# Performance work log

Hardware: AMD Instinct MI355X
Metric: run time of the kernel (lower is better)

## Reference

```python
import jax, jax.numpy as jnp
import numpy as np

N = 50000
E = 800000
G_DIM = 128
HEADS = 8
DEPTH = 3
EPS = 1e-5


def _ln(x, w, b):
    m = jnp.mean(x, axis=-1, keepdims=True)
    v = jnp.var(x, axis=-1, keepdims=True)
    return (x - m) * jax.lax.rsqrt(v + EPS) * w + b


def setup_inputs() -> dict:
    key = jax.random.key(0)
    ks = jax.random.split(key, 12)
    s = 0.02
    inp = {
        "h": jax.random.normal(ks[0], (N, G_DIM), jnp.float32),
        "src": jax.random.randint(ks[1], (E,), 0, N, jnp.int32),
        "dst": jax.random.randint(ks[2], (E,), 0, N, jnp.int32),
        # outer norm
        "norm_w": jnp.ones((G_DIM,), jnp.float32),
        "norm_b": jnp.zeros((G_DIM,), jnp.float32),
        # attention norm_in
        "nin_w": jnp.ones((G_DIM,), jnp.float32),
        "nin_b": jnp.zeros((G_DIM,), jnp.float32),
        # to_qkv (no bias)
        "Wqkv": jax.random.normal(ks[3], (G_DIM, 3 * G_DIM), jnp.float32) * s,
        # ff norm_out
        "no_w": jnp.ones((G_DIM,), jnp.float32),
        "no_b": jnp.zeros((G_DIM,), jnp.float32),
        # ff linears (hidden = 4*g_dim)
        "W1": jax.random.normal(ks[4], (G_DIM, 4 * G_DIM), jnp.float32) * s,
        "b1": jnp.zeros((4 * G_DIM,), jnp.float32),
        "W2": jax.random.normal(ks[5], (4 * G_DIM, G_DIM), jnp.float32) * s,
        "b2": jnp.zeros((G_DIM,), jnp.float32),
    }
    return inp


def _graph_attention(x, src, dst, nin_w, nin_b, Wqkv):
    # x: [N, g_dim]
    s = _ln(x, nin_w, nin_b)
    qkv = s @ Wqkv                                   # [N, 3*g_dim]
    q, k, v = jnp.split(qkv, 3, axis=-1)
    D = G_DIM // HEADS
    q = q.reshape(N, HEADS, D)
    k = k.reshape(N, HEADS, D)
    v = v.reshape(N, HEADS, D)
    scale = G_DIM ** (-0.5)
    # edge scores: elementwise q[src] * k[dst] per (head, dim) channel
    att = q[src] * k[dst] * scale                    # [E, H, D]
    # edge softmax over incoming edges of each dst node, per channel
    mx = jax.ops.segment_max(att, dst, num_segments=N)   # [N, H, D]
    e = jnp.exp(att - mx[dst])
    z = jax.ops.segment_sum(e, dst, num_segments=N)      # [N, H, D]
    a = e / z[dst]
    # weighted message aggregation
    rst = jax.ops.segment_sum(v[src] * a, dst, num_segments=N)  # [N, H, D]
    return rst.reshape(N, G_DIM)


def reference(h, src, dst, norm_w, norm_b, nin_w, nin_b, Wqkv,
              no_w, no_b, W1, b1, W2, b2):
    for _ in range(DEPTH):
        x = _ln(h, norm_w, norm_b)
        x = _graph_attention(x, src, dst, nin_w, nin_b, Wqkv)
        # feedforward with its own pre-norm
        y = _ln(x, no_w, no_b)
        y = jax.nn.gelu(y @ W1 + b1, approximate=False) @ W2 + b2
        h = y + h
    return h
```

## Files before the change

kernel.cpp:

```cpp
#include <hip/hip_runtime.h>
#include <math.h>

#define N_NODES 50000
#define N_EDGES 800000
#define EPS 1e-5f

typedef unsigned short u16;
typedef __attribute__((ext_vector_type(8))) u16 u16x8;
typedef __attribute__((ext_vector_type(8))) short bf16x8;
typedef __attribute__((ext_vector_type(4))) float f32x4;

__device__ __forceinline__ u16 f2bf(float x) {
  unsigned u = __float_as_uint(x);
  return (u16)((u + 0x7FFFu + ((u >> 16) & 1u)) >> 16);
}
__device__ __forceinline__ float bf2f(u16 b) {
  return __uint_as_float(((unsigned)b) << 16);
}

__global__ void count_kernel(const int* __restrict__ dst, int* __restrict__ cnt, int e_total) {
  int e = blockIdx.x * 256 + threadIdx.x;
  if (e < e_total) atomicAdd(&cnt[dst[e]], 1);
}

__global__ void scan_kernel(const int* __restrict__ cnt, int* __restrict__ offs,
                            int* __restrict__ cursor, int n) {
  __shared__ int buf[1024];
  int t = threadIdx.x;
  int chunk = (n + 1023) >> 10;
  int lo = t * chunk, hi = min(lo + chunk, n);
  int s = 0;
  for (int i = lo; i < hi; ++i) s += cnt[i];
  buf[t] = s;
  __syncthreads();
  for (int st = 1; st < 1024; st <<= 1) {
    int v = (t >= st) ? buf[t - st] : 0;
    __syncthreads();
    buf[t] += v;
    __syncthreads();
  }
  int run = (t == 0) ? 0 : buf[t - 1];
  for (int i = lo; i < hi; ++i) {
    int c = cnt[i];
    offs[i] = run; cursor[i] = run;
    run += c;
  }
  if (lo < n && hi == n) offs[n] = run;
}

__global__ void scatter_kernel(const int* __restrict__ src, const int* __restrict__ dst,
                               int* __restrict__ cursor, int* __restrict__ ssrc, int e_total) {
  int e = blockIdx.x * 256 + threadIdx.x;
  if (e < e_total) {
    int p = atomicAdd(&cursor[dst[e]], 1);
    ssrc[p] = src[e];
  }
}

__global__ void wsplit_kernel(const float* __restrict__ W, u16* __restrict__ outH,
                              u16* __restrict__ outL, int K, int M) {
  int e = blockIdx.x * 256 + threadIdx.x;
  if (e >= K * M) return;
  int n = e % M, k = e / M;
  float a = W[e];
  u16 hb = f2bf(a);
  outH[(size_t)n * K + k] = hb;
  outL[(size_t)n * K + k] = f2bf(a - bf2f(hb));
}

__device__ __forceinline__ float wave_sum(float v) {
#pragma unroll
  for (int m = 32; m > 0; m >>= 1) v += __shfl_xor(v, m, 64);
  return v;
}

__global__ __launch_bounds__(256) void ln2_kernel(
    const float* __restrict__ h,
    const float* __restrict__ w1, const float* __restrict__ b1,
    const float* __restrict__ w2, const float* __restrict__ b2,
    u16* __restrict__ s_hi, u16* __restrict__ s_lo, int n) {
  int lane = threadIdx.x & 63;
  int row = blockIdx.x * 4 + (threadIdx.x >> 6);
  if (row >= n) return;
  float2 v = ((const float2*)(h + (size_t)row * 128))[lane];
  float s = wave_sum(v.x + v.y);
  float q = wave_sum(v.x * v.x + v.y * v.y);
  float mean = s * (1.0f / 128.0f);
  float var = q * (1.0f / 128.0f) - mean * mean;
  float rs = 1.0f / sqrtf(var + EPS);
  float2 wv = ((const float2*)w1)[lane];
  float2 bv = ((const float2*)b1)[lane];
  float x0 = (v.x - mean) * rs * wv.x + bv.x;
  float x1 = (v.y - mean) * rs * wv.y + bv.y;
  float s2 = wave_sum(x0 + x1);
  float q2 = wave_sum(x0 * x0 + x1 * x1);
  float mean2 = s2 * (1.0f / 128.0f);
  float var2 = q2 * (1.0f / 128.0f) - mean2 * mean2;
  float rs2 = 1.0f / sqrtf(var2 + EPS);
  float2 wv2 = ((const float2*)w2)[lane];
  float2 bv2 = ((const float2*)b2)[lane];
  float o0 = (x0 - mean2) * rs2 * wv2.x + bv2.x;
  float o1 = (x1 - mean2) * rs2 * wv2.y + bv2.y;
  u16 h0 = f2bf(o0), h1 = f2bf(o1);
  u16 l0 = f2bf(o0 - bf2f(h0)), l1 = f2bf(o1 - bf2f(h1));
  ((unsigned*)s_hi)[(size_t)row * 64 + lane] = (unsigned)h0 | ((unsigned)h1 << 16);
  ((unsigned*)s_lo)[(size_t)row * 64 + lane] = (unsigned)l0 | ((unsigned)l1 << 16);
}

__global__ __launch_bounds__(256) void ln1_kernel(
    const float* __restrict__ h,
    const float* __restrict__ w1, const float* __restrict__ b1,
    u16* __restrict__ s_hi, u16* __restrict__ s_lo, int n) {
  int lane = threadIdx.x & 63;
  int row = blockIdx.x * 4 + (threadIdx.x >> 6);
  if (row >= n) return;
  float2 v = ((const float2*)(h + (size_t)row * 128))[lane];
  float s = wave_sum(v.x + v.y);
  float q = wave_sum(v.x * v.x + v.y * v.y);
  float mean = s * (1.0f / 128.0f);
  float var = q * (1.0f / 128.0f) - mean * mean;
  float rs = 1.0f / sqrtf(var + EPS);
  float2 wv = ((const float2*)w1)[lane];
  float2 bv = ((const float2*)b1)[lane];
  float o0 = (v.x - mean) * rs * wv.x + bv.x;
  float o1 = (v.y - mean) * rs * wv.y + bv.y;
  u16 h0 = f2bf(o0), h1 = f2bf(o1);
  u16 l0 = f2bf(o0 - bf2f(h0)), l1 = f2bf(o1 - bf2f(h1));
  ((unsigned*)s_hi)[(size_t)row * 64 + lane] = (unsigned)h0 | ((unsigned)h1 << 16);
  ((unsigned*)s_lo)[(size_t)row * 64 + lane] = (unsigned)l0 | ((unsigned)l1 << 16);
}

__global__ __launch_bounds__(256) void attn_kernel(
    const u16* __restrict__ qv, const float* __restrict__ kbuf,
    const int* __restrict__ offs, const int* __restrict__ ssrc,
    float* __restrict__ rst, int n) {
  int lane = threadIdx.x & 63;
  int node = blockIdx.x * 4 + (threadIdx.x >> 6);
  if (node >= n) return;
  const float SCALE = 0.08838834764831845f;
  float2 kc = ((const float2*)(kbuf + (size_t)node * 128))[lane];
  kc.x *= SCALE; kc.y *= SCALE;
  int e0 = offs[node], e1 = offs[node + 1];
  float z0 = 0.f, z1 = 0.f, a0 = 0.f, a1 = 0.f;
  int e = e0;
  for (; e + 1 < e1; e += 2) {
    int s0 = ssrc[e], s1 = ssrc[e + 1];
    ushort4 wa = ((const ushort4*)(qv + (size_t)s0 * 256))[lane];
    ushort4 wb = ((const ushort4*)(qv + (size_t)s1 * 256))[lane];
    float pa0 = __expf(bf2f(wa.x) * kc.x), pa1 = __expf(bf2f(wa.y) * kc.y);
    float pb0 = __expf(bf2f(wb.x) * kc.x), pb1 = __expf(bf2f(wb.y) * kc.y);
    z0 += pa0 + pb0;
    z1 += pa1 + pb1;
    a0 = fmaf(pa0, bf2f(wa.z), fmaf(pb0, bf2f(wb.z), a0));
    a1 = fmaf(pa1, bf2f(wa.w), fmaf(pb1, bf2f(wb.w), a1));
  }
  if (e < e1) {
    int s0 = ssrc[e];
    ushort4 wa = ((const ushort4*)(qv + (size_t)s0 * 256))[lane];
    float pa0 = __expf(bf2f(wa.x) * kc.x), pa1 = __expf(bf2f(wa.y) * kc.y);
    z0 += pa0; z1 += pa1;
    a0 = fmaf(pa0, bf2f(wa.z), a0);
    a1 = fmaf(pa1, bf2f(wa.w), a1);
  }
  float2 o;
  o.x = (e1 > e0) ? a0 / z0 : 0.f;
  o.y = (e1 > e0) ? a1 / z1 : 0.f;
  ((float2*)(rst + (size_t)node * 128))[lane] = o;
}

template <int ACT, bool SPLITA>
__global__ __launch_bounds__(256) void gemm_split(
    const u16* __restrict__ Ah, const u16* __restrict__ Al,
    const u16* __restrict__ BhT, const u16* __restrict__ BlT,
    const float* __restrict__ bias, const float* __restrict__ res,
    float* __restrict__ outF, u16* __restrict__ outH,
    u16* __restrict__ qvb, float* __restrict__ kbuf,
    int nrows, int K, int M) {
  __shared__ u16 Ae[128][72];
  __shared__ u16 Be[128][72];
  int tid = threadIdx.x;
  int lane = tid & 63;
  int wid = tid >> 6;
  int wr = wid >> 1, wc = wid & 1;
  int lr = lane & 15, lg = lane >> 4;
  int row0 = blockIdx.y * 128, col0 = blockIdx.x * 128;
  bool full_tile = (row0 + 128 <= nrows);

  f32x4 acc[4][4] = {};

  int ra0 = tid >> 2;
  int ka0 = (tid & 3) * 8;

  for (int k0 = 0; k0 < K; k0 += 32) {
    __syncthreads();
    if (full_tile) {
      int gr = row0 + ra0;
      *(u16x8*)&Ae[ra0][ka0]      = *(const u16x8*)(Ah + (size_t)gr * K + k0 + ka0);
      *(u16x8*)&Ae[ra0 + 64][ka0] = *(const u16x8*)(Ah + (size_t)(gr + 64) * K + k0 + ka0);
      if (SPLITA) {
        *(u16x8*)&Ae[ra0][32 + ka0]      = *(const u16x8*)(Al + (size_t)gr * K + k0 + ka0);
        *(u16x8*)&Ae[ra0 + 64][32 + ka0] = *(const u16x8*)(Al + (size_t)(gr + 64) * K + k0 + ka0);
      }
    } else {
      int gr = row0 + ra0;
      u16x8 h8 = {}, l8 = {};
      if (gr < nrows) {
        h8 = *(const u16x8*)(Ah + (size_t)gr * K + k0 + ka0);
        if (SPLITA) l8 = *(const u16x8*)(Al + (size_t)gr * K + k0 + ka0);
      }
      *(u16x8*)&Ae[ra0][ka0] = h8;
      if (SPLITA) *(u16x8*)&Ae[ra0][32 + ka0] = l8;
      gr += 64;
      u16x8 h8b = {}, l8b = {};
      if (gr < nrows) {
        h8b = *(const u16x8*)(Ah + (size_t)gr * K + k0 + ka0);
        if (SPLITA) l8b = *(const u16x8*)(Al + (size_t)gr * K + k0 + ka0);
      }
      *(u16x8*)&Ae[ra0 + 64][ka0] = h8b;
      if (SPLITA) *(u16x8*)&Ae[ra0 + 64][32 + ka0] = l8b;
    }
    {
      int gc = col0 + ra0;
      *(u16x8*)&Be[ra0][ka0]           = *(const u16x8*)(BhT + (size_t)gc * K + k0 + ka0);
      *(u16x8*)&Be[ra0][32 + ka0]      = *(const u16x8*)(BlT + (size_t)gc * K + k0 + ka0);
      *(u16x8*)&Be[ra0 + 64][ka0]      = *(const u16x8*)(BhT + (size_t)(gc + 64) * K + k0 + ka0);
      *(u16x8*)&Be[ra0 + 64][32 + ka0] = *(const u16x8*)(BlT + (size_t)(gc + 64) * K + k0 + ka0);
    }
    __syncthreads();

    bf16x8 afh[4], afl[4], bfh[4], bfl[4];
#pragma unroll
    for (int mi = 0; mi < 4; ++mi) {
      afh[mi] = *(const bf16x8*)&Ae[wr * 64 + mi * 16 + lr][lg * 8];
      if (SPLITA) afl[mi] = *(const bf16x8*)&Ae[wr * 64 + mi * 16 + lr][32 + lg * 8];
    }
#pragma unroll
    for (int ni = 0; ni < 4; ++ni) {
      bfh[ni] = *(const bf16x8*)&Be[wc * 64 + ni * 16 + lr][lg * 8];
      bfl[ni] = *(const bf16x8*)&Be[wc * 64 + ni * 16 + lr][32 + lg * 8];
    }
#pragma unroll
    for (int mi = 0; mi < 4; ++mi)
#pragma unroll
      for (int ni = 0; ni < 4; ++ni) {
        acc[mi][ni] = __builtin_amdgcn_mfma_f32_16x16x32_bf16(afh[mi], bfh[ni], acc[mi][ni], 0, 0, 0);
        if (SPLITA)
          acc[mi][ni] = __builtin_amdgcn_mfma_f32_16x16x32_bf16(afl[mi], bfh[ni], acc[mi][ni], 0, 0, 0);
        acc[mi][ni] = __builtin_amdgcn_mfma_f32_16x16x32_bf16(afh[mi], bfl[ni], acc[mi][ni], 0, 0, 0);
      }
  }

#pragma unroll
  for (int mi = 0; mi < 4; ++mi) {
#pragma unroll
    for (int j = 0; j < 4; ++j) {
      int r = row0 + wr * 64 + mi * 16 + lg * 4 + j;
      if (!full_tile && r >= nrows) continue;
#pragma unroll
      for (int ni = 0; ni < 4; ++ni) {
        int c = col0 + wc * 64 + ni * 16 + lr;
        float v = acc[mi][ni][j];
        if (ACT == 0) {
          if (c < 128) {
            qvb[(size_t)r * 256 + ((c >> 1) << 2) + (c & 1)] = f2bf(v);
          } else if (c < 256) {
            kbuf[(size_t)r * 128 + (c - 128)] = v;
          } else {
            int cc = c - 256;
            qvb[(size_t)r * 256 + ((cc >> 1) << 2) + 2 + (cc & 1)] = f2bf(v);
          }
        } else if (ACT == 1) {
          v += bias[c];
          v = 0.5f * v * (1.0f + erff(v * 0.70710678118654752f));
          outH[(size_t)r * M + c] = f2bf(v);
        } else {
          v += bias[c] + res[(size_t)r * M + c];
          outF[(size_t)r * M + c] = v;
        }
      }
    }
  }
}

extern "C" void kernel_launch(void* const* d_in, const int* in_sizes, int n_in,
                              void* d_out, int out_size, void* d_ws, size_t ws_size,
                              hipStream_t stream) {
  const float* h_in   = (const float*)d_in[0];
  const int*   src    = (const int*)d_in[1];
  const int*   dst    = (const int*)d_in[2];
  const float* norm_w = (const float*)d_in[3];
  const float* norm_b = (const float*)d_in[4];
  const float* nin_w  = (const float*)d_in[5];
  const float* nin_b  = (const float*)d_in[6];
  const float* Wqkv   = (const float*)d_in[7];
  const float* no_w   = (const float*)d_in[8];
  const float* no_b   = (const float*)d_in[9];
  const float* W1     = (const float*)d_in[10];
  const float* b1     = (const float*)d_in[11];
  const float* W2     = (const float*)d_in[12];
  const float* b2     = (const float*)d_in[13];
  float* out = (float*)d_out;

  char* wsp = (char*)d_ws;
  float* h_cur = (float*)wsp;             wsp += (size_t)N_NODES * 128 * 4;
  u16* s_hi = (u16*)wsp;                  wsp += (size_t)N_NODES * 128 * 2;
  u16* s_lo = (u16*)wsp;                  wsp += (size_t)N_NODES * 128 * 2;
  u16* qvb  = (u16*)wsp;                  wsp += (size_t)N_NODES * 256 * 2;
  float* kbuf = (float*)wsp;              wsp += (size_t)N_NODES * 128 * 4;
  u16* hid  = (u16*)wsp;                  wsp += (size_t)N_NODES * 512 * 2;
  u16* WqT_h = (u16*)wsp; wsp += 49152 * 2;
  u16* WqT_l = (u16*)wsp; wsp += 49152 * 2;
  u16* W1T_h = (u16*)wsp; wsp += 65536 * 2;
  u16* W1T_l = (u16*)wsp; wsp += 65536 * 2;
  u16* W2T_h = (u16*)wsp; wsp += 65536 * 2;
  u16* W2T_l = (u16*)wsp; wsp += 65536 * 2;
  int* cnt    = (int*)wsp;
  int* cursor = cnt + N_NODES;
  int* offs   = cursor + N_NODES;
  int* ssrc   = offs + N_NODES + 1;

  hipMemsetAsync(cnt, 0, N_NODES * sizeof(int), stream);
  count_kernel<<<(N_EDGES + 255) / 256, 256, 0, stream>>>(dst, cnt, N_EDGES);
  scan_kernel<<<1, 1024, 0, stream>>>(cnt, offs, cursor, N_NODES);
  scatter_kernel<<<(N_EDGES + 255) / 256, 256, 0, stream>>>(src, dst, cursor, ssrc, N_EDGES);

  wsplit_kernel<<<(128 * 384 + 255) / 256, 256, 0, stream>>>(Wqkv, WqT_h, WqT_l, 128, 384);
  wsplit_kernel<<<(128 * 512 + 255) / 256, 256, 0, stream>>>(W1, W1T_h, W1T_l, 128, 512);
  wsplit_kernel<<<(512 * 128 + 255) / 256, 256, 0, stream>>>(W2, W2T_h, W2T_l, 512, 128);

  const int grid_rows = (N_NODES + 127) / 128;

  for (int layer = 0; layer < 3; ++layer) {
    const float* h_src = (layer == 0) ? h_in : h_cur;
    float* h_dst = (layer == 2) ? out : h_cur;

    ln2_kernel<<<12500, 256, 0, stream>>>(h_src, norm_w, norm_b, nin_w, nin_b, s_hi, s_lo, N_NODES);
    gemm_split<0, true><<<dim3(3, grid_rows), 256, 0, stream>>>(
        s_hi, s_lo, WqT_h, WqT_l, nullptr, nullptr,
        nullptr, nullptr, qvb, kbuf, N_NODES, 128, 384);
    attn_kernel<<<12500, 256, 0, stream>>>(qvb, kbuf, offs, ssrc, out, N_NODES);
    ln1_kernel<<<12500, 256, 0, stream>>>(out, no_w, no_b, s_hi, s_lo, N_NODES);
    gemm_split<1, true><<<dim3(4, grid_rows), 256, 0, stream>>>(
        s_hi, s_lo, W1T_h, W1T_l, b1, nullptr,
        nullptr, hid, nullptr, nullptr, N_NODES, 128, 512);
    gemm_split<2, false><<<dim3(1, grid_rows), 256, 0, stream>>>(
        hid, nullptr, W2T_h, W2T_l, b2, h_src,
        h_dst, nullptr, nullptr, nullptr, N_NODES, 512, 128);
  }
}
```

Baseline: 981.4 us.

## Double-buffer GEMM LDS tiles with register prefetch and parallelize CSR scan

```diff
diff --git a/kernel.cpp b/kernel.cpp
--- a/kernel.cpp
+++ b/kernel.cpp
@@ -4,6 +4,9 @@
 #define N_NODES 50000
 #define N_EDGES 800000
 #define EPS 1e-5f
+
+#define SCAN_CHUNK 1024
+#define SCAN_NBLK ((N_NODES + SCAN_CHUNK - 1) / SCAN_CHUNK)
 
 typedef unsigned short u16;
 typedef __attribute__((ext_vector_type(8))) u16 u16x8;
@@ -23,29 +26,61 @@
   if (e < e_total) atomicAdd(&cnt[dst[e]], 1);
 }
 
-__global__ void scan_kernel(const int* __restrict__ cnt, int* __restrict__ offs,
-                            int* __restrict__ cursor, int n) {
-  __shared__ int buf[1024];
+__global__ __launch_bounds__(256) void scan1_kernel(const int* __restrict__ cnt,
+                                                    int* __restrict__ offs,
+                                                    int* __restrict__ bsum, int n) {
+  __shared__ int buf[256];
   int t = threadIdx.x;
-  int chunk = (n + 1023) >> 10;
-  int lo = t * chunk, hi = min(lo + chunk, n);
-  int s = 0;
-  for (int i = lo; i < hi; ++i) s += cnt[i];
-  buf[t] = s;
+  int base = blockIdx.x * SCAN_CHUNK + t * 4;
+  int v0 = (base + 0 < n) ? cnt[base + 0] : 0;
+  int v1 = (base + 1 < n) ? cnt[base + 1] : 0;
+  int v2 = (base + 2 < n) ? cnt[base + 2] : 0;
+  int v3 = (base + 3 < n) ? cnt[base + 3] : 0;
+  int tsum = v0 + v1 + v2 + v3;
+  buf[t] = tsum;
   __syncthreads();
-  for (int st = 1; st < 1024; st <<= 1) {
-    int v = (t >= st) ? buf[t - st] : 0;
+  for (int st = 1; st < 256; st <<= 1) {
+    int x = (t >= st) ? buf[t - st] : 0;
     __syncthreads();
-    buf[t] += v;
+    buf[t] += x;
     __syncthreads();
   }
-  int run = (t == 0) ? 0 : buf[t - 1];
-  for (int i = lo; i < hi; ++i) {
-    int c = cnt[i];
-    offs[i] = run; cursor[i] = run;
-    run += c;
-  }
-  if (lo < n && hi == n) offs[n] = run;
+  int texcl = buf[t] - tsum;
+  if (base + 0 < n) offs[base + 0] = texcl;
+  if (base + 1 < n) offs[base + 1] = texcl + v0;
+  if (base + 2 < n) offs[base + 2] = texcl + v0 + v1;
+  if (base + 3 < n) offs[base + 3] = texcl + v0 + v1 + v2;
+  if (t == 255) bsum[blockIdx.x] = buf[255];
+}
+
+__global__ void scan2_kernel(const int* __restrict__ bsum, int* __restrict__ bbase) {
+  int lane = threadIdx.x;
+  int v = (lane < SCAN_NBLK) ? bsum[lane] : 0;
+  int orig = v;
+#pragma unroll
+  for (int ofs = 1; ofs < 64; ofs <<= 1) {
+    int u = __shfl_up(v, ofs, 64);
+    if (lane >= ofs) v += u;
+  }
+  if (lane < SCAN_NBLK) bbase[lane] = v - orig;
+}
+
+__global__ __launch_bounds__(256) void scan3_kernel(int* __restrict__ offs,
+                                                    int* __restrict__ cursor,
+                                                    const int* __restrict__ bbase, int n) {
+  int t = threadIdx.x;
+  int b = bbase[blockIdx.x];
+  int base = blockIdx.x * SCAN_CHUNK + t * 4;
+#pragma unroll
+  for (int j = 0; j < 4; ++j) {
+    int i = base + j;
+    if (i < n) {
+      int o = offs[i] + b;
+      offs[i] = o;
+      cursor[i] = o;
+    }
+  }
+  if (blockIdx.x == 0 && t == 0) offs[n] = N_EDGES;
 }
 
 __global__ void scatter_kernel(const int* __restrict__ src, const int* __restrict__ dst,
@@ -168,16 +203,19 @@
   ((float2*)(rst + (size_t)node * 128))[lane] = o;
 }
 
-template <int ACT, bool SPLITA>
+struct StageA { u16x8 a0h, a1h, a0l, a1l; };
+struct StageB { u16x8 b0h, b0l, b1h, b1l; };
+
+template <int ACT, bool SPLITA, int K>
 __global__ __launch_bounds__(256) void gemm_split(
     const u16* __restrict__ Ah, const u16* __restrict__ Al,
     const u16* __restrict__ BhT, const u16* __restrict__ BlT,
     const float* __restrict__ bias, const float* __restrict__ res,
     float* __restrict__ outF, u16* __restrict__ outH,
     u16* __restrict__ qvb, float* __restrict__ kbuf,
-    int nrows, int K, int M) {
-  __shared__ u16 Ae[128][72];
-  __shared__ u16 Be[128][72];
+    int nrows, int M) {
+  __shared__ u16 Ae[2][128][72];
+  __shared__ u16 Be[2][128][72];
   int tid = threadIdx.x;
   int lane = tid & 63;
   int wid = tid >> 6;
@@ -191,53 +229,72 @@
   int ra0 = tid >> 2;
   int ka0 = (tid & 3) * 8;
 
-  for (int k0 = 0; k0 < K; k0 += 32) {
-    __syncthreads();
+  const int NT = K / 32;
+
+  auto loadA = [&](int k0, StageA& r) {
     if (full_tile) {
       int gr = row0 + ra0;
-      *(u16x8*)&Ae[ra0][ka0]      = *(const u16x8*)(Ah + (size_t)gr * K + k0 + ka0);
-      *(u16x8*)&Ae[ra0 + 64][ka0] = *(const u16x8*)(Ah + (size_t)(gr + 64) * K + k0 + ka0);
+      r.a0h = *(const u16x8*)(Ah + (size_t)gr * K + k0 + ka0);
+      r.a1h = *(const u16x8*)(Ah + (size_t)(gr + 64) * K + k0 + ka0);
       if (SPLITA) {
-        *(u16x8*)&Ae[ra0][32 + ka0]      = *(const u16x8*)(Al + (size_t)gr * K + k0 + ka0);
-        *(u16x8*)&Ae[ra0 + 64][32 + ka0] = *(const u16x8*)(Al + (size_t)(gr + 64) * K + k0 + ka0);
+        r.a0l = *(const u16x8*)(Al + (size_t)gr * K + k0 + ka0);
+        r.a1l = *(const u16x8*)(Al + (size_t)(gr + 64) * K + k0 + ka0);
       }
     } else {
       int gr = row0 + ra0;
-      u16x8 h8 = {}, l8 = {};
+      r.a0h = (u16x8){}; r.a1h = (u16x8){}; r.a0l = (u16x8){}; r.a1l = (u16x8){};
       if (gr < nrows) {
-        h8 = *(const u16x8*)(Ah + (size_t)gr * K + k0 + ka0);
-        if (SPLITA) l8 = *(const u16x8*)(Al + (size_t)gr * K + k0 + ka0);
+        r.a0h = *(const u16x8*)(Ah + (size_t)gr * K + k0 + ka0);
+        if (SPLITA) r.a0l = *(const u16x8*)(Al + (size_t)gr * K + k0 + ka0);
       }
-      *(u16x8*)&Ae[ra0][ka0] = h8;
-      if (SPLITA) *(u16x8*)&Ae[ra0][32 + ka0] = l8;
-      gr += 64;
-      u16x8 h8b = {}, l8b = {};
-      if (gr < nrows) {
-        h8b = *(const u16x8*)(Ah + (size_t)gr * K + k0 + ka0);
-        if (SPLITA) l8b = *(const u16x8*)(Al + (size_t)gr * K + k0 + ka0);
+      if (gr + 64 < nrows) {
+        r.a1h = *(const u16x8*)(Ah + (size_t)(gr + 64) * K + k0 + ka0);
+        if (SPLITA) r.a1l = *(const u16x8*)(Al + (size_t)(gr + 64) * K + k0 + ka0);
       }
-      *(u16x8*)&Ae[ra0 + 64][ka0] = h8b;
-      if (SPLITA) *(u16x8*)&Ae[ra0 + 64][32 + ka0] = l8b;
-    }
-    {
-      int gc = col0 + ra0;
-      *(u16x8*)&Be[ra0][ka0]           = *(const u16x8*)(BhT + (size_t)gc * K + k0 + ka0);
-      *(u16x8*)&Be[ra0][32 + ka0]      = *(const u16x8*)(BlT + (size_t)gc * K + k0 + ka0);
-      *(u16x8*)&Be[ra0 + 64][ka0]      = *(const u16x8*)(BhT + (size_t)(gc + 64) * K + k0 + ka0);
-      *(u16x8*)&Be[ra0 + 64][32 + ka0] = *(const u16x8*)(BlT + (size_t)(gc + 64) * K + k0 + ka0);
-    }
-    __syncthreads();
-
+    }
+  };
+  auto loadB = [&](int k0, StageB& r) {
+    int gc = col0 + ra0;
+    r.b0h = *(const u16x8*)(BhT + (size_t)gc * K + k0 + ka0);
+    r.b0l = *(const u16x8*)(BlT + (size_t)gc * K + k0 + ka0);
+    r.b1h = *(const u16x8*)(BhT + (size_t)(gc + 64) * K + k0 + ka0);
+    r.b1l = *(const u16x8*)(BlT + (size_t)(gc + 64) * K + k0 + ka0);
+  };
+  auto writeLDS = [&](int buf, const StageA& a, const StageB& b) {
+    *(u16x8*)&Ae[buf][ra0][ka0] = a.a0h;
+    *(u16x8*)&Ae[buf][ra0 + 64][ka0] = a.a1h;
+    if (SPLITA) {
+      *(u16x8*)&Ae[buf][ra0][32 + ka0] = a.a0l;
+      *(u16x8*)&Ae[buf][ra0 + 64][32 + ka0] = a.a1l;
+    }
+    *(u16x8*)&Be[buf][ra0][ka0] = b.b0h;
+    *(u16x8*)&Be[buf][ra0][32 + ka0] = b.b0l;
+    *(u16x8*)&Be[buf][ra0 + 64][ka0] = b.b1h;
+    *(u16x8*)&Be[buf][ra0 + 64][32 + ka0] = b.b1l;
+  };
+
+  StageA ar; StageB br;
+  loadA(0, ar); loadB(0, br);
+  writeLDS(0, ar, br);
+  __syncthreads();
+
+#pragma unroll
+  for (int t = 0; t < NT; ++t) {
+    int cur = t & 1;
+    if (t + 1 < NT) {
+      loadA((t + 1) * 32, ar);
+      loadB((t + 1) * 32, br);
+    }
     bf16x8 afh[4], afl[4], bfh[4], bfl[4];
 #pragma unroll
     for (int mi = 0; mi < 4; ++mi) {
-      afh[mi] = *(const bf16x8*)&Ae[wr * 64 + mi * 16 + lr][lg * 8];
-      if (SPLITA) afl[mi] = *(const bf16x8*)&Ae[wr * 64 + mi * 16 + lr][32 + lg * 8];
+      afh[mi] = *(const bf16x8*)&Ae[cur][wr * 64 + mi * 16 + lr][lg * 8];
+      if (SPLITA) afl[mi] = *(const bf16x8*)&Ae[cur][wr * 64 + mi * 16 + lr][32 + lg * 8];
     }
 #pragma unroll
     for (int ni = 0; ni < 4; ++ni) {
-      bfh[ni] = *(const bf16x8*)&Be[wc * 64 + ni * 16 + lr][lg * 8];
-      bfl[ni] = *(const bf16x8*)&Be[wc * 64 + ni * 16 + lr][32 + lg * 8];
+      bfh[ni] = *(const bf16x8*)&Be[cur][wc * 64 + ni * 16 + lr][lg * 8];
+      bfl[ni] = *(const bf16x8*)&Be[cur][wc * 64 + ni * 16 + lr][32 + lg * 8];
     }
 #pragma unroll
     for (int mi = 0; mi < 4; ++mi)
@@ -248,6 +305,8 @@
           acc[mi][ni] = __builtin_amdgcn_mfma_f32_16x16x32_bf16(afl[mi], bfh[ni], acc[mi][ni], 0, 0, 0);
         acc[mi][ni] = __builtin_amdgcn_mfma_f32_16x16x32_bf16(afh[mi], bfl[ni], acc[mi][ni], 0, 0, 0);
       }
+    if (t + 1 < NT) writeLDS(cur ^ 1, ar, br);
+    __syncthreads();
   }
 
 #pragma unroll
@@ -318,10 +377,14 @@
   int* cursor = cnt + N_NODES;
   int* offs   = cursor + N_NODES;
   int* ssrc   = offs + N_NODES + 1;
+  int* bsum   = ssrc + N_EDGES;
+  int* bbase  = bsum + 64;
 
   hipMemsetAsync(cnt, 0, N_NODES * sizeof(int), stream);
   count_kernel<<<(N_EDGES + 255) / 256, 256, 0, stream>>>(dst, cnt, N_EDGES);
-  scan_kernel<<<1, 1024, 0, stream>>>(cnt, offs, cursor, N_NODES);
+  scan1_kernel<<<SCAN_NBLK, 256, 0, stream>>>(cnt, offs, bsum, N_NODES);
+  scan2_kernel<<<1, 64, 0, stream>>>(bsum, bbase);
+  scan3_kernel<<<SCAN_NBLK, 256, 0, stream>>>(offs, cursor, bbase, N_NODES);
   scatter_kernel<<<(N_EDGES + 255) / 256, 256, 0, stream>>>(src, dst, cursor, ssrc, N_EDGES);
 
   wsplit_kernel<<<(128 * 384 + 255) / 256, 256, 0, stream>>>(Wqkv, WqT_h, WqT_l, 128, 384);
@@ -335,16 +398,16 @@
     float* h_dst = (layer == 2) ? out : h_cur;
 
     ln2_kernel<<<12500, 256, 0, stream>>>(h_src, norm_w, norm_b, nin_w, nin_b, s_hi, s_lo, N_NODES);
-    gemm_split<0, true><<<dim3(3, grid_rows), 256, 0, stream>>>(
+    gemm_split<0, true, 128><<<dim3(3, grid_rows), 256, 0, stream>>>(
         s_hi, s_lo, WqT_h, WqT_l, nullptr, nullptr,
-        nullptr, nullptr, qvb, kbuf, N_NODES, 128, 384);
+        nullptr, nullptr, qvb, kbuf, N_NODES, 384);
     attn_kernel<<<12500, 256, 0, stream>>>(qvb, kbuf, offs, ssrc, out, N_NODES);
     ln1_kernel<<<12500, 256, 0, stream>>>(out, no_w, no_b, s_hi, s_lo, N_NODES);
-    gemm_split<1, true><<<dim3(4, grid_rows), 256, 0, stream>>>(
+    gemm_split<1, true, 128><<<dim3(4, grid_rows), 256, 0, stream>>>(
         s_hi, s_lo, W1T_h, W1T_l, b1, nullptr,
-        nullptr, hid, nullptr, nullptr, N_NODES, 128, 512);
-    gemm_split<2, false><<<dim3(1, grid_rows), 256, 0, stream>>>(
+        nullptr, hid, nullptr, nullptr, N_NODES, 512);
+    gemm_split<2, false, 512><<<dim3(1, grid_rows), 256, 0, stream>>>(
         hid, nullptr, W2T_h, W2T_l, b2, h_src,
-        h_dst, nullptr, nullptr, nullptr, N_NODES, 512, 128);
-  }
-}
+        h_dst, nullptr, nullptr, nullptr, N_NODES, 128);
+  }
+}
```

Result: faster. 861.7 us (-12.2%).
